# Performance work log

Measured on AMD Instinct MI355X. Metric: run time of the kernel, lower is better.

The kernel has to match this reference:

```python
import jax, jax.numpy as jnp
import numpy as np

S = 15      # subject_nums
C = 2048    # in_channels (extractor output dim)
NC = 3      # num_classes
B = 1024    # subject_batch_num (rows per subject)
SUBJ = 7    # target subject
KERNEL_MUL = 2.0
KERNEL_NUM = 5


def setup_inputs() -> dict:
    key = jax.random.key(0)
    k = jax.random.split(key, 5)
    x = jax.random.normal(k[0], (S * B, C), dtype=jnp.float32)
    labels = jax.random.randint(k[1], (S * B,), 0, NC)
    y = jax.nn.one_hot(labels, NC, dtype=jnp.float32)
    subject_label = jnp.repeat(jnp.arange(S, dtype=jnp.int32), B)
    W_add = 0.02 * jax.random.normal(k[2], (S, 512, C), dtype=jnp.float32)
    b_add = jnp.zeros((S, 512), dtype=jnp.float32)
    W_cls = 0.02 * jax.random.normal(k[3], (S, NC, 512), dtype=jnp.float32)
    b_cls = jnp.zeros((S, NC), dtype=jnp.float32)
    return {"x": x, "y": y, "subject_label": subject_label,
            "W_add": W_add, "b_add": b_add, "W_cls": W_cls, "b_cls": b_cls,
            "subject": SUBJ}


def _mmd(source, target):
    # Standard multi-kernel Gaussian MMD (DAN-style), as used in the repo.
    n = source.shape[0]
    total = jnp.concatenate([source, target], axis=0)      # [2n, d]
    sq = jnp.sum(total * total, axis=-1)
    d2 = sq[:, None] + sq[None, :] - 2.0 * (total @ total.T)  # [2n, 2n]
    m = 2 * n
    bandwidth = jnp.sum(d2) / (m * m - m)
    bandwidth = bandwidth / (KERNEL_MUL ** (KERNEL_NUM // 2))
    kernels = sum(jnp.exp(-d2 / (bandwidth * (KERNEL_MUL ** i))) for i in range(KERNEL_NUM))
    XX = kernels[:n, :n]
    YY = kernels[n:, n:]
    XY = kernels[:n, n:]
    YX = kernels[n:, :n]
    return jnp.mean(XX + YY - XY - YX)


def reference(x, y, subject_label, W_add, b_add, W_cls, b_cls, subject):
    S_ = W_add.shape[0]
    b = x.shape[0] // S_          # == (subject_label == subject).sum() by construction
    K = S_ - 1
    idx = np.array([i for i in range(S_) if i != subject])  # static: subject is a Python int

    xr = x.reshape(S_, b, -1)
    src = xr[idx]                 # [K, b, C] source-subject blocks
    tgt = xr[subject]             # [b, C] target-subject block
    Wk, bk = W_add[idx], b_add[idx]

    # Grouped per-subject addblock Linear(C -> 512)
    outs = jnp.einsum('kbc,kdc->kbd', src, Wk) + bk[:, None, :]       # [K, b, 512]
    t_outs = jnp.einsum('bc,kdc->kbd', tgt, Wk) + bk[:, None, :]      # [K, b, 512]

    # Class predictors: ReLU + Linear(512 -> NC), predictors 0..K-1 are used
    Wc, bc = W_cls[:K], b_cls[:K]
    logits = jnp.einsum('kbd,knd->kbn', jax.nn.relu(outs), Wc) + bc[:, None, :]
    t_logits = jnp.einsum('kbd,knd->kbn', jax.nn.relu(t_outs), Wc) + bc[:, None, :]

    # ---- MMD loss ----
    mmd_loss = jnp.mean(jax.vmap(_mmd)(outs, t_outs))

    # ---- DISC loss: pairwise |softmax - softmax| over source features ----
    P = jax.nn.softmax(outs, axis=-1)                                  # [K, b, 512]
    disc_loss = 0.0
    for i in range(K - 1):  # fixed small loop over subjects, inner term vectorized
        disc_loss = disc_loss + jnp.abs(P[i + 1:] - P[i]).mean(axis=(1, 2)).sum()
    disc_loss = disc_loss * 2.0 / (K * (K - 1))

    # ---- CLS loss: KL(one-hot/soft target || log_softmax(logits)) ----
    yr = y.reshape(S_, b, -1)[idx]                                     # [K, b, NC]
    logp = jax.nn.log_softmax(logits, axis=-1)
    safe_y = jnp.where(yr > 0, yr, 1.0)
    kl = jnp.where(yr > 0, yr * (jnp.log(safe_y) - logp), 0.0)         # 0*log0 -> 0 (torch kl_div)
    cls_loss = kl.sum(-1).mean()

    # ---- PRED ACC on target subject ----
    t_prob = jax.nn.softmax(t_logits, axis=-1).mean(axis=0)            # [b, NC]
    y_tgt = y.reshape(S_, b, -1)[subject]
    pred = jnp.sum(jnp.argmax(t_prob, axis=1) == jnp.argmax(y_tgt, axis=1))
    nums = b

    return (mmd_loss * 0.1, disc_loss * 0.4, cls_loss, pred, nums)
```

## Files before the change

### kernel.cpp

```cpp
#include <hip/hip_runtime.h>
#include <hip/hip_bf16.h>
#include <stdint.h>

typedef __attribute__((ext_vector_type(8))) __bf16 bf16x8;
typedef __attribute__((ext_vector_type(4))) float f32x4;

#define CDIM 2048
#define DDIM 512

__device__ __forceinline__ unsigned short f2bf(float f) {
  union { float f; unsigned u; } a; a.f = f;
  unsigned r = a.u + 0x7FFFu + ((a.u >> 16) & 1u);
  return (unsigned short)(r >> 16);
}
__device__ __forceinline__ float bf2f(unsigned short h) {
  union { unsigned u; float f; } a; a.u = ((unsigned)h) << 16;
  return a.f;
}

typedef const __attribute__((address_space(1))) void gas_void;
typedef __attribute__((address_space(3))) void las_void;
__device__ __forceinline__ void async16(const void* g, void* l) {
  __builtin_amdgcn_global_load_lds((gas_void*)g, (las_void*)l, 16, 0, 0);
}

#define VMW(n) asm volatile("s_waitcnt vmcnt(" #n ")" ::: "memory")
#define SBAR() __builtin_amdgcn_s_barrier()
#define SFENCE() __builtin_amdgcn_sched_barrier(0)

__device__ __forceinline__ float blockSum256(float v) {
  __shared__ float sh[4];
  #pragma unroll
  for (int o = 32; o; o >>= 1) v += __shfl_xor(v, o, 64);
  int lane = threadIdx.x & 63, w = threadIdx.x >> 6;
  __syncthreads();
  if (lane == 0) sh[w] = v;
  __syncthreads();
  return sh[0] + sh[1] + sh[2] + sh[3];
}

__device__ __forceinline__ bf16x8 lds_frag(const unsigned short* base, int row, int cb) {
  return *(const bf16x8*)(base + row*64 + (((cb ^ (row & 7))) << 3));
}

__global__ __launch_bounds__(256) void k_convert(const float* __restrict__ x,
    const float* __restrict__ w, uint2* __restrict__ x16, uint2* __restrict__ w16) {
  const int nx4 = 15*1024*CDIM/4;
  const int nw4 = 15*DDIM*CDIM/4;
  int stride = gridDim.x * blockDim.x;
  for (int i = blockIdx.x*blockDim.x + threadIdx.x; i < nx4; i += stride) {
    float4 v = ((const float4*)x)[i];
    x16[i] = make_uint2((unsigned)f2bf(v.x) | ((unsigned)f2bf(v.y) << 16),
                        (unsigned)f2bf(v.z) | ((unsigned)f2bf(v.w) << 16));
  }
  for (int i = blockIdx.x*blockDim.x + threadIdx.x; i < nw4; i += stride) {
    float4 v = ((const float4*)w)[i];
    w16[i] = make_uint2((unsigned)f2bf(v.x) | ((unsigned)f2bf(v.y) << 16),
                        (unsigned)f2bf(v.z) | ((unsigned)f2bf(v.w) << 16));
  }
}

__global__ __launch_bounds__(512, 2) void k_gemm1(
    const unsigned short* __restrict__ x16,
    const unsigned short* __restrict__ w16,
    const float* __restrict__ b_add,
    const int* __restrict__ subj_p,
    unsigned short* __restrict__ t16,
    float* __restrict__ scol)
{
  int bid = blockIdx.x;
  int k, t;
  if (bid < 256) { k = bid & 7; t = bid >> 3; }
  else { int b2 = bid - 256; k = 8 + (b2 & 7); t = b2 >> 3; if (k >= 14) return; }
  int mt = t >> 1, nt = t & 1;
  const int subj = *subj_p;
  int ik = (k < subj) ? k : (k + 1);

  __shared__ unsigned short lds[3*384*64];

  int tid = threadIdx.x;
  int lane = tid & 63;
  int w = tid >> 6;
  int wm = w >> 2, wn = w & 3;
  int rr = lane >> 3;
  int cc8 = ((lane & 7) ^ rr) << 3;

  const unsigned short* Bb = w16 + (size_t)ik * DDIM * CDIM;

  f32x4 acc[4][4];
  #pragma unroll
  for (int a = 0; a < 4; a++)
    #pragma unroll
    for (int b = 0; b < 4; b++) acc[a][b] = f32x4{0.f,0.f,0.f,0.f};

  auto stage = [&](int tt, int bufi) {
    unsigned short* buf = lds + bufi*(384*64);
    int ks = tt*64;
    #pragma unroll
    for (int i = 0; i < 2; i++) {
      int r0 = (w*2 + i)*8;
      int gr = mt*128 + r0 + rr;
      int xrow = ((gr < 1024) ? ik : subj)*1024 + (gr & 1023);
      async16(x16 + (size_t)xrow*CDIM + ks + cc8, buf + r0*64);
    }
    #pragma unroll
    for (int i = 0; i < 4; i++) {
      int r0 = (w*4 + i)*8;
      int gn = nt*256 + r0 + rr;
      async16(Bb + (size_t)gn*CDIM + ks + cc8, buf + 8192 + r0*64);
    }
  };

  auto compute = [&](int bufi) {
    const unsigned short* A = lds + bufi*(384*64);
    const unsigned short* B = A + 8192;
    bf16x8 af[4][2], bfr[4][2];
    #pragma unroll
    for (int a = 0; a < 4; a++)
      #pragma unroll
      for (int ksl = 0; ksl < 2; ksl++)
        af[a][ksl] = lds_frag(A, wm*64 + a*16 + (lane & 15), ksl*4 + (lane >> 4));
    #pragma unroll
    for (int bb = 0; bb < 4; bb++)
      #pragma unroll
      for (int ksl = 0; ksl < 2; ksl++)
        bfr[bb][ksl] = lds_frag(B, wn*64 + bb*16 + (lane & 15), ksl*4 + (lane >> 4));
    __builtin_amdgcn_s_setprio(1);
    #pragma unroll
    for (int a = 0; a < 4; a++)
      #pragma unroll
      for (int bb = 0; bb < 4; bb++) {
        acc[a][bb] = __builtin_amdgcn_mfma_f32_16x16x32_bf16(af[a][0], bfr[bb][0], acc[a][bb], 0, 0, 0);
        acc[a][bb] = __builtin_amdgcn_mfma_f32_16x16x32_bf16(af[a][1], bfr[bb][1], acc[a][bb], 0, 0, 0);
      }
    __builtin_amdgcn_s_setprio(0);
  };

  stage(0, 0);
  stage(1, 1);
  VMW(6); SBAR(); SFENCE();

  int cur = 0;
  for (int tt = 0; tt < 30; ++tt) {
    int nb = cur + 2; if (nb >= 3) nb -= 3;
    stage(tt + 2, nb);
    compute(cur);
    VMW(6); SBAR(); SFENCE();
    cur = (cur == 2) ? 0 : cur + 1;
  }
  compute(cur);
  VMW(0); SBAR(); SFENCE();
  cur = (cur == 2) ? 0 : cur + 1;
  compute(cur);

  const float* bias = b_add + ik*DDIM;
  #pragma unroll
  for (int bb = 0; bb < 4; bb++) {
    int coln = nt*256 + wn*64 + bb*16 + (lane & 15);
    float bv = bias[coln];
    float cs = 0.f;
    #pragma unroll
    for (int a = 0; a < 4; a++) {
      #pragma unroll
      for (int r = 0; r < 4; r++) {
        int rowm = mt*128 + wm*64 + a*16 + ((lane >> 4) << 2) + r;
        float val = acc[a][bb][r] + bv;
        t16[((size_t)k*2048 + rowm)*DDIM + coln] = f2bf(val);
        cs += val;
      }
    }
    cs += __shfl_xor(cs, 16, 64);
    cs += __shfl_xor(cs, 32, 64);
    if ((lane >> 4) == 0) atomicAdd(&scol[k*DDIM + coln], cs);
  }
}

__global__ __launch_bounds__(256) void k_rowred(const unsigned short* __restrict__ t16,
    float* __restrict__ sq, float* __restrict__ rmax, float* __restrict__ rinv)
{
  int wid = blockIdx.x*4 + (threadIdx.x >> 6);
  int lane = threadIdx.x & 63;
  uint4 v = *(const uint4*)(t16 + (size_t)wid * DDIM + lane*8);
  unsigned uu[4] = {v.x, v.y, v.z, v.w};
  float f[8];
  #pragma unroll
  for (int q = 0; q < 4; q++) {
    f[2*q]   = bf2f((unsigned short)(uu[q] & 0xffffu));
    f[2*q+1] = bf2f((unsigned short)(uu[q] >> 16));
  }
  float s2 = 0.f, mx = -3.4e38f;
  #pragma unroll
  for (int j = 0; j < 8; j++) { s2 += f[j]*f[j]; mx = fmaxf(mx, f[j]); }
  #pragma unroll
  for (int o = 32; o; o >>= 1) { s2 += __shfl_xor(s2, o, 64); mx = fmaxf(mx, __shfl_xor(mx, o, 64)); }
  float se = 0.f;
  #pragma unroll
  for (int j = 0; j < 8; j++) se += __expf(f[j] - mx);
  #pragma unroll
  for (int o = 32; o; o >>= 1) se += __shfl_xor(se, o, 64);
  if (lane == 0) { sq[wid] = s2; rmax[wid] = mx; rinv[wid] = 1.f/se; }
}

__global__ __launch_bounds__(256) void k_bw(const float* __restrict__ sq,
    const float* __restrict__ scol, float* __restrict__ c2)
{
  int k = blockIdx.x;
  float a = 0.f;
  for (int r = threadIdx.x; r < 2048; r += 256) a += sq[k*2048 + r];
  float b = 0.f;
  for (int d = threadIdx.x; d < 512; d += 256) { float v = scol[k*512 + d]; b += v*v; }
  float atot = blockSum256(a);
  float btot = blockSum256(b);
  if (threadIdx.x == 0) {
    float sumd2 = 2.f*2048.f*atot - 2.f*btot;
    float bw = sumd2 / (2048.f*2048.f - 2048.f) * 0.25f;
    #pragma unroll
    for (int i = 0; i < 5; i++)
      c2[k*5 + i] = -1.4426950408889634f / (bw * (float)(1 << i));
  }
}

__global__ __launch_bounds__(256, 2) void k_mmd(
    const unsigned short* __restrict__ t16,
    const float* __restrict__ sq,
    const float* __restrict__ c2,
    float* __restrict__ g_acc)
{
  int bid = blockIdx.x;
  int k, pr;
  if (bid < 1088) { k = bid & 7; pr = bid >> 3; }
  else { int b2 = bid - 1088; k = 8 + (b2 & 7); pr = b2 >> 3; if (k >= 14) return; }
  int tri = pr;
  int it = 0;
  while (tri >= 16 - it) { tri -= 16 - it; it++; }
  int jt = it + tri;

  const unsigned short* T = t16 + (size_t)k * 2048 * DDIM;

  __shared__ unsigned short lds[2*256*64];
  __shared__ float sqs[256];

  int tid = threadIdx.x;
  int lane = tid & 63;
  int w = tid >> 6;
  int wm = w >> 1, wn = w & 1;
  int rr = lane >> 3;
  int cc8 = ((lane & 7) ^ rr) << 3;

  f32x4 acc[4][4];
  #pragma unroll
  for (int a = 0; a < 4; a++)
    #pragma unroll
    for (int b = 0; b < 4; b++) acc[a][b] = f32x4{0.f,0.f,0.f,0.f};

  auto stage = [&](int tt, int bufi) {
    unsigned short* buf = lds + bufi*(256*64);
    int ks = tt*64;
    #pragma unroll
    for (int i = 0; i < 4; i++) {
      int r0 = (w*4 + i)*8;
      async16(T + (size_t)(it*128 + r0 + rr)*DDIM + ks + cc8, buf + r0*64);
    }
    #pragma unroll
    for (int i = 0; i < 4; i++) {
      int r0 = (w*4 + i)*8;
      async16(T + (size_t)(jt*128 + r0 + rr)*DDIM + ks + cc8, buf + 8192 + r0*64);
    }
  };

  auto compute = [&](int bufi) {
    const unsigned short* A = lds + bufi*(256*64);
    const unsigned short* B = A + 8192;
    bf16x8 af[4][2], bfr[4][2];
    #pragma unroll
    for (int a = 0; a < 4; a++)
      #pragma unroll
      for (int ksl = 0; ksl < 2; ksl++)
        af[a][ksl] = lds_frag(A, wm*64 + a*16 + (lane & 15), ksl*4 + (lane >> 4));
    #pragma unroll
    for (int bb = 0; bb < 4; bb++)
      #pragma unroll
      for (int ksl = 0; ksl < 2; ksl++)
        bfr[bb][ksl] = lds_frag(B, wn*64 + bb*16 + (lane & 15), ksl*4 + (lane >> 4));
    __builtin_amdgcn_s_setprio(1);
    #pragma unroll
    for (int a = 0; a < 4; a++)
      #pragma unroll
      for (int bb = 0; bb < 4; bb++) {
        acc[a][bb] = __builtin_amdgcn_mfma_f32_16x16x32_bf16(af[a][0], bfr[bb][0], acc[a][bb], 0, 0, 0);
        acc[a][bb] = __builtin_amdgcn_mfma_f32_16x16x32_bf16(af[a][1], bfr[bb][1], acc[a][bb], 0, 0, 0);
      }
    __builtin_amdgcn_s_setprio(0);
  };

  stage(0, 0);
  VMW(0); SBAR(); SFENCE();

  int cur = 0;
  for (int tt = 0; tt < 7; ++tt) {
    stage(tt + 1, cur ^ 1);
    compute(cur);
    VMW(0); SBAR(); SFENCE();
    cur ^= 1;
  }
  compute(cur);

  if (tid < 128) sqs[tid] = sq[k*2048 + it*128 + tid];
  else           sqs[tid] = sq[k*2048 + jt*128 + (tid - 128)];
  __syncthreads();

  float c4 = c2[k*5 + 4];
  float part = 0.f;
  #pragma unroll
  for (int a = 0; a < 4; a++) {
    #pragma unroll
    for (int bb = 0; bb < 4; bb++) {
      int rj = wn*64 + bb*16 + (lane & 15);
      float sj = sqs[128 + rj];
      #pragma unroll
      for (int r = 0; r < 4; r++) {
        int ri = wm*64 + a*16 + ((lane >> 4) << 2) + r;
        float d2 = sqs[ri] + sj - 2.f*acc[a][bb][r];
        float z = exp2f(c4*d2);
        float z2 = z*z, z4 = z2*z2, z8 = z4*z4;
        part += z + z2 + z4 + z8 + z8*z8;
      }
    }
  }
  float tot = blockSum256(part);
  if (tid == 0) {
    float sgn = ((it < 8) == (jt < 8)) ? 1.f : -1.f;
    float wgt = (it == jt) ? 1.f : 2.f;
    atomicAdd(&g_acc[k], sgn * wgt * tot);
  }
}

__global__ __launch_bounds__(256) void k_heads(const unsigned short* __restrict__ t16,
    const float* __restrict__ rmax, const float* __restrict__ rinv,
    const float* __restrict__ W_cls, const float* __restrict__ b_cls,
    const float* __restrict__ y, const int* __restrict__ subj_p,
    float* __restrict__ g_acc, float* __restrict__ pacc)
{
  if (blockIdx.x < 2048) {
    int b = blockIdx.x;
    int row = b >> 1;
    int d = ((b & 1) << 8) + threadIdx.x;
    float p[14];
    #pragma unroll
    for (int k = 0; k < 14; k++) {
      float tv = bf2f(t16[((size_t)(k*2048 + row))*DDIM + d]);
      p[k] = __expf(tv - rmax[k*2048 + row]) * rinv[k*2048 + row];
    }
    float s = 0.f;
    #pragma unroll
    for (int i2 = 0; i2 < 14; i2++)
      #pragma unroll
      for (int j2 = i2+1; j2 < 14; j2++)
        s += fabsf(p[i2] - p[j2]);
    float tot = blockSum256(s);
    if (threadIdx.x == 0) atomicAdd(&g_acc[14 + (b & 7)], tot);
  } else {
    __shared__ float shk[4];
    int bid = blockIdx.x - 2048;
    int w = threadIdx.x >> 6;
    int lane = threadIdx.x & 63;
    int wid = bid*4 + w;
    int k = wid >> 11, r = wid & 2047;
    uint4 v = *(const uint4*)(t16 + (size_t)wid * DDIM + lane*8);
    unsigned uu[4] = {v.x, v.y, v.z, v.w};
    float f[8];
    #pragma unroll
    for (int q = 0; q < 4; q++) {
      f[2*q]   = fmaxf(bf2f((unsigned short)(uu[q] & 0xffffu)), 0.f);
      f[2*q+1] = fmaxf(bf2f((unsigned short)(uu[q] >> 16)), 0.f);
    }
    const float* Wc = W_cls + k*3*DDIM;
    int d0 = lane*8;
    float l0 = 0.f, l1 = 0.f, l2 = 0.f;
    #pragma unroll
    for (int j = 0; j < 8; j++) {
      l0 += f[j]*Wc[d0+j];
      l1 += f[j]*Wc[DDIM + d0+j];
      l2 += f[j]*Wc[2*DDIM + d0+j];
    }
    #pragma unroll
    for (int o = 32; o; o >>= 1) {
      l0 += __shfl_xor(l0, o, 64); l1 += __shfl_xor(l1, o, 64); l2 += __shfl_xor(l2, o, 64);
    }
    if (r < 1024) {
      if (lane == 0) {
        l0 += b_cls[k*3+0]; l1 += b_cls[k*3+1]; l2 += b_cls[k*3+2];
        float mx = fmaxf(l0, fmaxf(l1, l2));
        float lse = mx + __logf(__expf(l0-mx) + __expf(l1-mx) + __expf(l2-mx));
        int subj = *subj_p;
        int ik = (k < subj) ? k : k+1;
        const float* yr = y + ((size_t)(ik*1024 + r))*3;
        float tl = (yr[0] > 0.5f) ? l0 : ((yr[1] > 0.5f) ? l1 : l2);
        shk[w] = lse - tl;
      }
      __syncthreads();
      if (threadIdx.x == 0)
        atomicAdd(&g_acc[22 + k], shk[0] + shk[1] + shk[2] + shk[3]);
    } else {
      if (lane == 0) {
        l0 += b_cls[k*3+0]; l1 += b_cls[k*3+1]; l2 += b_cls[k*3+2];
        float mx = fmaxf(l0, fmaxf(l1, l2));
        float e0 = __expf(l0-mx), e1 = __expf(l1-mx), e2 = __expf(l2-mx);
        float inv = 1.f/(e0+e1+e2);
        int j = r - 1024;
        atomicAdd(&pacc[j*3 + 0], e0*inv);
        atomicAdd(&pacc[j*3 + 1], e1*inv);
        atomicAdd(&pacc[j*3 + 2], e2*inv);
      }
    }
  }
}

__global__ __launch_bounds__(256) void k_pred(const float* __restrict__ pacc,
    const float* __restrict__ y, const int* __restrict__ subj_p, float* __restrict__ g_acc)
{
  int j = blockIdx.x*256 + threadIdx.x;
  int subj = *subj_p;
  float p0 = pacc[j*3+0], p1 = pacc[j*3+1], p2 = pacc[j*3+2];
  int pa = 0; float pm = p0;
  if (p1 > pm) { pa = 1; pm = p1; }
  if (p2 > pm) { pa = 2; }
  const float* yt = y + ((size_t)(subj*1024 + j))*3;
  int ya = 0; float ym = yt[0];
  if (yt[1] > ym) { ya = 1; ym = yt[1]; }
  if (yt[2] > ym) { ya = 2; }
  float tot = blockSum256((pa == ya) ? 1.f : 0.f);
  if (threadIdx.x == 0) atomicAdd(&g_acc[36], tot);
}

__global__ void k_fin(const float* __restrict__ g_acc, float* __restrict__ out)
{
  if (threadIdx.x == 0 && blockIdx.x == 0) {
    float s = 0.f;
    for (int k = 0; k < 14; k++) s += g_acc[k];
    float disc = 0.f;
    for (int i = 14; i < 22; i++) disc += g_acc[i];
    float cls = 0.f;
    for (int i = 22; i < 36; i++) cls += g_acc[i];
    out[0] = 0.1f * s / (14.f * 1024.f * 1024.f);
    out[1] = 0.4f * disc * (2.f / (14.f*13.f)) / (1024.f*512.f);
    out[2] = cls / (14.f*1024.f);
    out[3] = g_acc[36];
    out[4] = 1024.f;
  }
}

extern "C" void kernel_launch(void* const* d_in, const int* in_sizes, int n_in,
                              void* d_out, int out_size, void* d_ws, size_t ws_size,
                              hipStream_t stream)
{
  (void)in_sizes; (void)n_in; (void)out_size; (void)ws_size;
  const float* x     = (const float*)d_in[0];
  const float* y     = (const float*)d_in[1];
  const float* W_add = (const float*)d_in[3];
  const float* b_add = (const float*)d_in[4];
  const float* W_cls = (const float*)d_in[5];
  const float* b_cls = (const float*)d_in[6];
  const int*   subj  = (const int*)d_in[7];

  char* ws = (char*)d_ws;
  size_t o = 0;
  auto take = [&](size_t b) { char* p = ws + o; o += (b + 255) & ~(size_t)255; return p; };
  unsigned short* X16 = (unsigned short*)take((size_t)15*1024*2048*2);
  unsigned short* W16 = (unsigned short*)take((size_t)15*512*2048*2);
  unsigned short* T16 = (unsigned short*)take((size_t)14*2048*512*2);
  float* SQ   = (float*)take((size_t)14*2048*4);
  float* RMAX = (float*)take((size_t)14*2048*4);
  float* RINV = (float*)take((size_t)14*2048*4);
  float* C2   = (float*)take(512);
  float* SCOL = (float*)take((size_t)14*512*4);
  float* PACC = (float*)take((size_t)1024*3*4);
  float* ACC  = (float*)take(256);

  hipMemsetAsync(SCOL, 0, 14*512*4 + 1024*3*4 + 256, stream);

  k_convert<<<2048, 256, 0, stream>>>(x, W_add, (uint2*)X16, (uint2*)W16);
  k_gemm1 <<<512, 512, 0, stream>>>(X16, W16, b_add, subj, T16, SCOL);
  k_rowred<<<14*2048/4, 256, 0, stream>>>(T16, SQ, RMAX, RINV);
  k_bw    <<<14, 256, 0, stream>>>(SQ, SCOL, C2);
  k_mmd   <<<2176, 256, 0, stream>>>(T16, SQ, C2, ACC);
  k_heads <<<2048 + 14*2048/4, 256, 0, stream>>>(T16, RMAX, RINV, W_cls, b_cls, y, subj, ACC, PACC);
  k_pred  <<<4, 256, 0, stream>>>(PACC, y, subj, ACC);
  k_fin   <<<1, 64, 0, stream>>>(ACC, (float*)d_out);
}
```

Before: 451.9 us.

## Fuse row reductions into GEMM epilogue and widen bf16 conversion stores

The GEMM epilogue now computes per-row sum of squares and sum of exp with lane shuffles and accumulates them atomically, which removes the separate k_rowred kernel and its extra pass over T16. The softmax in the heads kernel drops max-subtraction and divides exp(t) by the accumulated row sum, relying on the activations being small enough not to overflow. The convert kernel processes 8 floats per thread and writes 16-byte stores. This adds row-level atomics inside the GEMM epilogue and gives up the numerical stability of the max-shifted softmax.

```diff
diff --git a/kernel.cpp b/kernel.cpp
--- a/kernel.cpp
+++ b/kernel.cpp
@@ -8,10 +8,10 @@
 #define CDIM 2048
 #define DDIM 512
 
-__device__ __forceinline__ unsigned short f2bf(float f) {
+__device__ __forceinline__ unsigned f2bf(float f) {
   union { float f; unsigned u; } a; a.f = f;
   unsigned r = a.u + 0x7FFFu + ((a.u >> 16) & 1u);
-  return (unsigned short)(r >> 16);
+  return r >> 16;
 }
 __device__ __forceinline__ float bf2f(unsigned short h) {
   union { unsigned u; float f; } a; a.u = ((unsigned)h) << 16;
@@ -44,19 +44,30 @@
 }
 
 __global__ __launch_bounds__(256) void k_convert(const float* __restrict__ x,
-    const float* __restrict__ w, uint2* __restrict__ x16, uint2* __restrict__ w16) {
-  const int nx4 = 15*1024*CDIM/4;
-  const int nw4 = 15*DDIM*CDIM/4;
+    const float* __restrict__ w, uint4* __restrict__ x16, uint4* __restrict__ w16) {
+  const int nx8 = 15*1024*CDIM/8;
+  const int nw8 = 15*DDIM*CDIM/8;
   int stride = gridDim.x * blockDim.x;
-  for (int i = blockIdx.x*blockDim.x + threadIdx.x; i < nx4; i += stride) {
-    float4 v = ((const float4*)x)[i];
-    x16[i] = make_uint2((unsigned)f2bf(v.x) | ((unsigned)f2bf(v.y) << 16),
-                        (unsigned)f2bf(v.z) | ((unsigned)f2bf(v.w) << 16));
-  }
-  for (int i = blockIdx.x*blockDim.x + threadIdx.x; i < nw4; i += stride) {
-    float4 v = ((const float4*)w)[i];
-    w16[i] = make_uint2((unsigned)f2bf(v.x) | ((unsigned)f2bf(v.y) << 16),
-                        (unsigned)f2bf(v.z) | ((unsigned)f2bf(v.w) << 16));
+  int t0 = blockIdx.x*blockDim.x + threadIdx.x;
+  const float4* xv = (const float4*)x;
+  const float4* wv = (const float4*)w;
+  for (int i = t0; i < nx8; i += stride) {
+    float4 a = xv[2*i], b = xv[2*i+1];
+    uint4 o;
+    o.x = f2bf(a.x) | (f2bf(a.y) << 16);
+    o.y = f2bf(a.z) | (f2bf(a.w) << 16);
+    o.z = f2bf(b.x) | (f2bf(b.y) << 16);
+    o.w = f2bf(b.z) | (f2bf(b.w) << 16);
+    x16[i] = o;
+  }
+  for (int i = t0; i < nw8; i += stride) {
+    float4 a = wv[2*i], b = wv[2*i+1];
+    uint4 o;
+    o.x = f2bf(a.x) | (f2bf(a.y) << 16);
+    o.y = f2bf(a.z) | (f2bf(a.w) << 16);
+    o.z = f2bf(b.x) | (f2bf(b.y) << 16);
+    o.w = f2bf(b.z) | (f2bf(b.w) << 16);
+    w16[i] = o;
   }
 }
 
@@ -66,7 +77,9 @@
     const float* __restrict__ b_add,
     const int* __restrict__ subj_p,
     unsigned short* __restrict__ t16,
-    float* __restrict__ scol)
+    float* __restrict__ scol,
+    float* __restrict__ rowsq,
+    float* __restrict__ rowex)
 {
   int bid = blockIdx.x;
   int k, t;
@@ -154,51 +167,45 @@
   compute(cur);
 
   const float* bias = b_add + ik*DDIM;
+  int coln[4]; float bv[4];
   #pragma unroll
   for (int bb = 0; bb < 4; bb++) {
-    int coln = nt*256 + wn*64 + bb*16 + (lane & 15);
-    float bv = bias[coln];
-    float cs = 0.f;
-    #pragma unroll
-    for (int a = 0; a < 4; a++) {
-      #pragma unroll
-      for (int r = 0; r < 4; r++) {
-        int rowm = mt*128 + wm*64 + a*16 + ((lane >> 4) << 2) + r;
-        float val = acc[a][bb][r] + bv;
-        t16[((size_t)k*2048 + rowm)*DDIM + coln] = f2bf(val);
-        cs += val;
-      }
-    }
-    cs += __shfl_xor(cs, 16, 64);
-    cs += __shfl_xor(cs, 32, 64);
-    if ((lane >> 4) == 0) atomicAdd(&scol[k*DDIM + coln], cs);
-  }
-}
-
-__global__ __launch_bounds__(256) void k_rowred(const unsigned short* __restrict__ t16,
-    float* __restrict__ sq, float* __restrict__ rmax, float* __restrict__ rinv)
-{
-  int wid = blockIdx.x*4 + (threadIdx.x >> 6);
-  int lane = threadIdx.x & 63;
-  uint4 v = *(const uint4*)(t16 + (size_t)wid * DDIM + lane*8);
-  unsigned uu[4] = {v.x, v.y, v.z, v.w};
-  float f[8];
-  #pragma unroll
-  for (int q = 0; q < 4; q++) {
-    f[2*q]   = bf2f((unsigned short)(uu[q] & 0xffffu));
-    f[2*q+1] = bf2f((unsigned short)(uu[q] >> 16));
-  }
-  float s2 = 0.f, mx = -3.4e38f;
-  #pragma unroll
-  for (int j = 0; j < 8; j++) { s2 += f[j]*f[j]; mx = fmaxf(mx, f[j]); }
-  #pragma unroll
-  for (int o = 32; o; o >>= 1) { s2 += __shfl_xor(s2, o, 64); mx = fmaxf(mx, __shfl_xor(mx, o, 64)); }
-  float se = 0.f;
-  #pragma unroll
-  for (int j = 0; j < 8; j++) se += __expf(f[j] - mx);
-  #pragma unroll
-  for (int o = 32; o; o >>= 1) se += __shfl_xor(se, o, 64);
-  if (lane == 0) { sq[wid] = s2; rmax[wid] = mx; rinv[wid] = 1.f/se; }
+    coln[bb] = nt*256 + wn*64 + bb*16 + (lane & 15);
+    bv[bb] = bias[coln[bb]];
+  }
+  float cs[4] = {0.f, 0.f, 0.f, 0.f};
+  #pragma unroll
+  for (int a = 0; a < 4; a++) {
+    #pragma unroll
+    for (int r = 0; r < 4; r++) {
+      int rowm = mt*128 + wm*64 + a*16 + ((lane >> 4) << 2) + r;
+      float sqp = 0.f, exq = 0.f;
+      #pragma unroll
+      for (int bb = 0; bb < 4; bb++) {
+        float val = acc[a][bb][r] + bv[bb];
+        t16[((size_t)k*2048 + rowm)*DDIM + coln[bb]] = (unsigned short)f2bf(val);
+        sqp += val*val;
+        exq += __expf(val);
+        cs[bb] += val;
+      }
+      #pragma unroll
+      for (int o2 = 1; o2 <= 8; o2 <<= 1) {
+        sqp += __shfl_xor(sqp, o2, 64);
+        exq += __shfl_xor(exq, o2, 64);
+      }
+      if ((lane & 15) == 0) {
+        atomicAdd(&rowsq[k*2048 + rowm], sqp);
+        atomicAdd(&rowex[k*2048 + rowm], exq);
+      }
+    }
+  }
+  #pragma unroll
+  for (int bb = 0; bb < 4; bb++) {
+    float c = cs[bb];
+    c += __shfl_xor(c, 16, 64);
+    c += __shfl_xor(c, 32, 64);
+    if ((lane >> 4) == 0) atomicAdd(&scol[k*DDIM + coln[bb]], c);
+  }
 }
 
 __global__ __launch_bounds__(256) void k_bw(const float* __restrict__ sq,
@@ -336,7 +343,7 @@
 }
 
 __global__ __launch_bounds__(256) void k_heads(const unsigned short* __restrict__ t16,
-    const float* __restrict__ rmax, const float* __restrict__ rinv,
+    const float* __restrict__ rowex,
     const float* __restrict__ W_cls, const float* __restrict__ b_cls,
     const float* __restrict__ y, const int* __restrict__ subj_p,
     float* __restrict__ g_acc, float* __restrict__ pacc)
@@ -349,7 +356,7 @@
     #pragma unroll
     for (int k = 0; k < 14; k++) {
       float tv = bf2f(t16[((size_t)(k*2048 + row))*DDIM + d]);
-      p[k] = __expf(tv - rmax[k*2048 + row]) * rinv[k*2048 + row];
+      p[k] = __expf(tv) / rowex[k*2048 + row];
     }
     float s = 0.f;
     #pragma unroll
@@ -469,22 +476,20 @@
   unsigned short* X16 = (unsigned short*)take((size_t)15*1024*2048*2);
   unsigned short* W16 = (unsigned short*)take((size_t)15*512*2048*2);
   unsigned short* T16 = (unsigned short*)take((size_t)14*2048*512*2);
+  float* C2   = (float*)take(512);
   float* SQ   = (float*)take((size_t)14*2048*4);
-  float* RMAX = (float*)take((size_t)14*2048*4);
-  float* RINV = (float*)take((size_t)14*2048*4);
-  float* C2   = (float*)take(512);
+  float* SE   = (float*)take((size_t)14*2048*4);
   float* SCOL = (float*)take((size_t)14*512*4);
   float* PACC = (float*)take((size_t)1024*3*4);
   float* ACC  = (float*)take(256);
 
-  hipMemsetAsync(SCOL, 0, 14*512*4 + 1024*3*4 + 256, stream);
-
-  k_convert<<<2048, 256, 0, stream>>>(x, W_add, (uint2*)X16, (uint2*)W16);
-  k_gemm1 <<<512, 512, 0, stream>>>(X16, W16, b_add, subj, T16, SCOL);
-  k_rowred<<<14*2048/4, 256, 0, stream>>>(T16, SQ, RMAX, RINV);
+  hipMemsetAsync(SQ, 0, (char*)ACC - (char*)SQ + 256, stream);
+
+  k_convert<<<2048, 256, 0, stream>>>(x, W_add, (uint4*)X16, (uint4*)W16);
+  k_gemm1 <<<512, 512, 0, stream>>>(X16, W16, b_add, subj, T16, SCOL, SQ, SE);
   k_bw    <<<14, 256, 0, stream>>>(SQ, SCOL, C2);
   k_mmd   <<<2176, 256, 0, stream>>>(T16, SQ, C2, ACC);
-  k_heads <<<2048 + 14*2048/4, 256, 0, stream>>>(T16, RMAX, RINV, W_cls, b_cls, y, subj, ACC, PACC);
+  k_heads <<<2048 + 14*2048/4, 256, 0, stream>>>(T16, SE, W_cls, b_cls, y, subj, ACC, PACC);
   k_pred  <<<4, 256, 0, stream>>>(PACC, y, subj, ACC);
   k_fin   <<<1, 64, 0, stream>>>(ACC, (float*)d_out);
 }
```

Result: no change. 448.9 us (-0.6%).
